# Optimization experiments

Measured on AMD Instinct MI355X. Metric: run time of the kernel, lower is better.

## Reference

```python
import jax, jax.numpy as jnp
import numpy as np
from jax import lax

B, T, H, H1 = 128, 512, 256, 128


def setup_inputs() -> dict:
    key = jax.random.key(0)
    ks = jax.random.split(key, 9)
    s = 1.0 / np.sqrt(H)  # torch LSTM/Linear init scale (uniform), use scaled normal for simplicity
    return {
        "x": jax.random.normal(ks[0], (B, T, 1), dtype=jnp.float32),
        "W_ih": jax.random.normal(ks[1], (4 * H, 1), dtype=jnp.float32) * s,
        "W_hh": jax.random.normal(ks[2], (4 * H, H), dtype=jnp.float32) * s,
        "b_ih": jax.random.normal(ks[3], (4 * H,), dtype=jnp.float32) * s,
        "b_hh": jax.random.normal(ks[4], (4 * H,), dtype=jnp.float32) * s,
        "W1": jax.random.normal(ks[5], (H1, H), dtype=jnp.float32) * s,
        "b1": jax.random.normal(ks[6], (H1,), dtype=jnp.float32) * s,
        "W2": jax.random.normal(ks[7], (1, H1), dtype=jnp.float32) / np.sqrt(H1),
        "b2": jax.random.normal(ks[8], (1,), dtype=jnp.float32) / np.sqrt(H1),
    }


def _lstm_last_hidden(x, W_ih, W_hh, b_ih, b_hh):
    # Precompute input contribution for all timesteps: [B,T,4H]
    xg = jnp.einsum("bti,gi->btg", x, W_ih) + (b_ih + b_hh)
    Bv, Hv = x.shape[0], W_hh.shape[1]
    h0 = jnp.zeros((Bv, Hv), dtype=x.dtype)
    c0 = jnp.zeros((Bv, Hv), dtype=x.dtype)

    def step(carry, xg_t):
        h, c = carry
        gates = xg_t + h @ W_hh.T  # [B,4H]
        i, f, g, o = jnp.split(gates, 4, axis=-1)  # torch gate order: i,f,g,o
        i = jax.nn.sigmoid(i)
        f = jax.nn.sigmoid(f)
        g = jnp.tanh(g)
        o = jax.nn.sigmoid(o)
        c = f * c + i * g
        h = o * jnp.tanh(c)
        return (h, c), None

    (h_last, _), _ = lax.scan(step, (h0, c0), jnp.swapaxes(xg, 0, 1))
    return h_last  # == lstm output at t=T-1 (x[:, -1, :] in torch)


def reference(x, W_ih, W_hh, b_ih, b_hh, W1, b1, W2, b2):
    h = _lstm_last_hidden(x, W_ih, W_hh, b_ih, b_hh)  # [B,H]
    y = jax.nn.relu(h @ W1.T + b1) @ W2.T + b2  # [B,1]
    return y
```

## Files before the change

kernel.cpp:

```cpp
#include <hip/hip_runtime.h>

#define TT 512
#define HH 256

typedef _Float16 half2t __attribute__((ext_vector_type(2)));

__device__ __forceinline__ float dot2acc(unsigned w, unsigned h, float acc) {
#if __has_builtin(__builtin_amdgcn_fdot2)
    return __builtin_amdgcn_fdot2(__builtin_bit_cast(half2t, w),
                                  __builtin_bit_cast(half2t, h), acc, false);
#else
    union U { unsigned u; _Float16 f[2]; };
    U uw, uh; uw.u = w; uh.u = h;
    acc = __builtin_fmaf((float)uw.f[0], (float)uh.f[0], acc);
    acc = __builtin_fmaf((float)uw.f[1], (float)uh.f[1], acc);
    return acc;
#endif
}

__device__ __forceinline__ unsigned packh2(float a, float b) {
    union U { _Float16 f[2]; unsigned u; } r;
    r.f[0] = (_Float16)a; r.f[1] = (_Float16)b;
    return r.u;
}

#define AGPR_W(dst, src) \
    asm volatile("v_accvgpr_write_b32 %0, %1" : "=a"(dst) : "v"(src))
#define AGPR_R(dst, src) \
    asm("v_accvgpr_read_b32 %0, %1" : "=v"(dst) : "a"(src))

__device__ __forceinline__ float qsum4(float v) {
    int a = __builtin_amdgcn_mov_dpp(__builtin_bit_cast(int, v), 0xB1, 0xF, 0xF, true);
    float r = v + __builtin_bit_cast(float, a);
    int b = __builtin_amdgcn_mov_dpp(__builtin_bit_cast(int, r), 0x4E, 0xF, 0xF, true);
    return r + __builtin_bit_cast(float, b);
}

__global__ __launch_bounds__(1024)
__attribute__((amdgpu_waves_per_eu(4, 4)))
void lstm_single(
    const float* __restrict__ x,
    const float* __restrict__ W_ih,
    const float* __restrict__ W_hh,
    const float* __restrict__ b_ih,
    const float* __restrict__ b_hh,
    const float* __restrict__ W1,
    const float* __restrict__ b1,
    const float* __restrict__ W2,
    const float* __restrict__ b2,
    float* __restrict__ out)
{
    const int b = blockIdx.x;
    const int j = threadIdx.x;
    const int e = j >> 2;
    const int s = j & 3;

    __shared__ __align__(16) unsigned wl[9][1024][4];
    __shared__ __align__(16) unsigned hbuf[2][140];
    __shared__ float h32[HH];
    __shared__ float x_lds[TT];
    __shared__ float red[128];

    unsigned wag[64];
    unsigned wv[28];
    #pragma unroll
    for (int g = 0; g < 4; ++g) {
        const float* pR = W_hh + (size_t)(g * 256 + e) * HH + 64 * s;
        #pragma unroll
        for (int k = 0; k < 16; ++k) {
            unsigned pw = packh2(pR[2 * k], pR[2 * k + 1]);
            AGPR_W(wag[g * 16 + k], pw);
        }
        #pragma unroll
        for (int k = 0; k < 7; ++k)
            wv[g * 7 + k] = packh2(pR[2 * (16 + k)], pR[2 * (16 + k) + 1]);
    }
    #pragma unroll
    for (int k = 0; k < 28; ++k)
        asm volatile("" : "+v"(wv[k]));
    #pragma unroll
    for (int u = 0; u < 9; ++u) {
        #pragma unroll
        for (int c2 = 0; c2 < 4; ++c2) {
            const int m = 4 * u + c2;
            const int g = m / 9, k = 23 + m % 9;
            const float* pR = W_hh + (size_t)(g * 256 + e) * HH + 64 * s;
            wl[u][j][c2] = packh2(pR[2 * k], pR[2 * k + 1]);
        }
    }

    float wih[4], bias[4];
    #pragma unroll
    for (int g = 0; g < 4; ++g) {
        const int R = g * 256 + e;
        wih[g]  = W_ih[R];
        bias[g] = b_ih[R] + b_hh[R];
    }

    if (j < TT) x_lds[j] = x[(size_t)b * TT + j];
    if (j < 140) { hbuf[0][j] = 0u; hbuf[1][j] = 0u; }
    float c = 0.0f;
    __syncthreads();

    for (int t = 0; t < TT; ++t) {
        const int p  = t & 1;
        const int pn = p ^ 1;
        const float xv = x_lds[t];
        const unsigned* hb = &hbuf[p][36 * s];
        float acc[4] = {0.f, 0.f, 0.f, 0.f};

        #pragma unroll
        for (int i = 0; i < 4; ++i) {
            uint4 hq = *reinterpret_cast<const uint4*>(&hb[4 * i]);
            #pragma unroll
            for (int g = 0; g < 4; ++g) {
                unsigned w0, w1, w2, w3;
                AGPR_R(w0, wag[g * 16 + 4 * i + 0]);
                AGPR_R(w1, wag[g * 16 + 4 * i + 1]);
                AGPR_R(w2, wag[g * 16 + 4 * i + 2]);
                AGPR_R(w3, wag[g * 16 + 4 * i + 3]);
                acc[g] = dot2acc(w0, hq.x, acc[g]);
                acc[g] = dot2acc(w1, hq.y, acc[g]);
                acc[g] = dot2acc(w2, hq.z, acc[g]);
                acc[g] = dot2acc(w3, hq.w, acc[g]);
            }
        }
        uint4 h4 = *reinterpret_cast<const uint4*>(&hb[16]);
        uint4 h5 = *reinterpret_cast<const uint4*>(&hb[20]);
        #pragma unroll
        for (int g = 0; g < 4; ++g) {
            acc[g] = dot2acc(wv[g * 7 + 0], h4.x, acc[g]);
            acc[g] = dot2acc(wv[g * 7 + 1], h4.y, acc[g]);
            acc[g] = dot2acc(wv[g * 7 + 2], h4.z, acc[g]);
            acc[g] = dot2acc(wv[g * 7 + 3], h4.w, acc[g]);
            acc[g] = dot2acc(wv[g * 7 + 4], h5.x, acc[g]);
            acc[g] = dot2acc(wv[g * 7 + 5], h5.y, acc[g]);
            acc[g] = dot2acc(wv[g * 7 + 6], h5.z, acc[g]);
        }
        uint4 h6 = *reinterpret_cast<const uint4*>(&hb[24]);
        uint4 h7 = *reinterpret_cast<const uint4*>(&hb[28]);
        const unsigned hw[9] = {h5.w, h6.x, h6.y, h6.z, h6.w,
                                h7.x, h7.y, h7.z, h7.w};
        #pragma unroll
        for (int u = 0; u < 9; ++u) {
            uint4 wq = *reinterpret_cast<const uint4*>(&wl[u][j][0]);
            { const int m = 4*u+0; acc[m/9] = dot2acc(wq.x, hw[m%9], acc[m/9]); }
            { const int m = 4*u+1; acc[m/9] = dot2acc(wq.y, hw[m%9], acc[m/9]); }
            { const int m = 4*u+2; acc[m/9] = dot2acc(wq.z, hw[m%9], acc[m/9]); }
            { const int m = 4*u+3; acc[m/9] = dot2acc(wq.w, hw[m%9], acc[m/9]); }
        }

        float gi = qsum4(acc[0]) + __builtin_fmaf(xv, wih[0], bias[0]);
        float gf = qsum4(acc[1]) + __builtin_fmaf(xv, wih[1], bias[1]);
        float gg = qsum4(acc[2]) + __builtin_fmaf(xv, wih[2], bias[2]);
        float go = qsum4(acc[3]) + __builtin_fmaf(xv, wih[3], bias[3]);

        gi = __builtin_amdgcn_rcpf(1.f + __expf(-gi));
        gf = __builtin_amdgcn_rcpf(1.f + __expf(-gf));
        go = __builtin_amdgcn_rcpf(1.f + __expf(-go));
        gg = 2.f * __builtin_amdgcn_rcpf(1.f + __expf(-2.f * gg)) - 1.f;
        c = __builtin_fmaf(gf, c, gi * gg);
        float th = 2.f * __builtin_amdgcn_rcpf(1.f + __expf(-2.f * c)) - 1.f;
        float hn = go * th;

        if ((e >> 6) == s)
            reinterpret_cast<unsigned short*>(&hbuf[pn][0])[e + 8 * s] =
                __builtin_bit_cast(unsigned short, (_Float16)hn);
        if (s == 0) h32[e] = hn;
        __syncthreads();
    }

    if (j < 128) {
        const float4* w1p = reinterpret_cast<const float4*>(W1 + (size_t)j * HH);
        const float4* hp  = reinterpret_cast<const float4*>(h32);
        float s0 = 0.f, s1 = 0.f, s2 = 0.f, s3 = 0.f;
        #pragma unroll
        for (int k = 0; k < 64; ++k) {
            float4 wv4 = w1p[k], hv = hp[k];
            s0 = __builtin_fmaf(wv4.x, hv.x, s0);
            s1 = __builtin_fmaf(wv4.y, hv.y, s1);
            s2 = __builtin_fmaf(wv4.z, hv.z, s2);
            s3 = __builtin_fmaf(wv4.w, hv.w, s3);
        }
        float rv = fmaxf((s0 + s1) + (s2 + s3) + b1[j], 0.f);
        red[j] = rv * W2[j];
    }
    __syncthreads();
    if (j == 0) {
        float y = b2[0];
        #pragma unroll 4
        for (int k = 0; k < 128; ++k) y += red[k];
        out[b] = y;
    }
}

extern "C" void kernel_launch(void* const* d_in, const int* in_sizes, int n_in,
                              void* d_out, int out_size, void* d_ws, size_t ws_size,
                              hipStream_t stream) {
    const float* x    = (const float*)d_in[0];
    const float* W_ih = (const float*)d_in[1];
    const float* W_hh = (const float*)d_in[2];
    const float* b_ih = (const float*)d_in[3];
    const float* b_hh = (const float*)d_in[4];
    const float* W1   = (const float*)d_in[5];
    const float* b1   = (const float*)d_in[6];
    const float* W2   = (const float*)d_in[7];
    const float* b2   = (const float*)d_in[8];
    float* out = (float*)d_out;

    lstm_single<<<128, 1024, 0, stream>>>(x, W_ih, W_hh, b_ih, b_hh,
                                          W1, b1, W2, b2, out);
}
```

Measured before the change: 1.172 ms.

## Move LDS-resident recurrent weight tail into global workspace with register prefetch

The 144KB slice of packed fp16 W_hh that was held in shared memory is now written to a global workspace buffer and streamed back each timestep, software-pipelined through four uint4 registers loaded at the top of the loop. The aim is to free LDS and cut the cost of LDS reads inside the recurrence. In exchange every step depends on L2/L1 loads that sit on the serial critical path, and 100KB of dynamic shared memory is requested but never used. All blocks write identical data to the same workspace locations, which is benign but redundant.

```diff
diff --git a/kernel.cpp b/kernel.cpp
--- a/kernel.cpp
+++ b/kernel.cpp
@@ -35,6 +35,14 @@
     int b = __builtin_amdgcn_mov_dpp(__builtin_bit_cast(int, r), 0x4E, 0xF, 0xF, true);
     return r + __builtin_bit_cast(float, b);
 }
+
+#define TCONS(TQ, U)                                                          \
+    do {                                                                      \
+        acc[(4*(U)+0)/9] = dot2acc((TQ).x, hw[(4*(U)+0)%9], acc[(4*(U)+0)/9]); \
+        acc[(4*(U)+1)/9] = dot2acc((TQ).y, hw[(4*(U)+1)%9], acc[(4*(U)+1)/9]); \
+        acc[(4*(U)+2)/9] = dot2acc((TQ).z, hw[(4*(U)+2)%9], acc[(4*(U)+2)/9]); \
+        acc[(4*(U)+3)/9] = dot2acc((TQ).w, hw[(4*(U)+3)%9], acc[(4*(U)+3)/9]); \
+    } while (0)
 
 __global__ __launch_bounds__(1024)
 __attribute__((amdgpu_waves_per_eu(4, 4)))
@@ -48,14 +56,14 @@
     const float* __restrict__ b1,
     const float* __restrict__ W2,
     const float* __restrict__ b2,
-    float* __restrict__ out)
+    float* __restrict__ out,
+    uint4* __restrict__ wt)
 {
     const int b = blockIdx.x;
     const int j = threadIdx.x;
     const int e = j >> 2;
     const int s = j & 3;
 
-    __shared__ __align__(16) unsigned wl[9][1024][4];
     __shared__ __align__(16) unsigned hbuf[2][140];
     __shared__ float h32[HH];
     __shared__ float x_lds[TT];
@@ -78,15 +86,31 @@
     #pragma unroll
     for (int k = 0; k < 28; ++k)
         asm volatile("" : "+v"(wv[k]));
+
     #pragma unroll
     for (int u = 0; u < 9; ++u) {
-        #pragma unroll
-        for (int c2 = 0; c2 < 4; ++c2) {
-            const int m = 4 * u + c2;
-            const int g = m / 9, k = 23 + m % 9;
-            const float* pR = W_hh + (size_t)(g * 256 + e) * HH + 64 * s;
-            wl[u][j][c2] = packh2(pR[2 * k], pR[2 * k + 1]);
-        }
+        uint4 v;
+        {
+            const int m = 4 * u + 0, g = m / 9, k = 23 + m % 9;
+            const float* pR = W_hh + (size_t)(g * 256 + e) * HH + 64 * s;
+            v.x = packh2(pR[2 * k], pR[2 * k + 1]);
+        }
+        {
+            const int m = 4 * u + 1, g = m / 9, k = 23 + m % 9;
+            const float* pR = W_hh + (size_t)(g * 256 + e) * HH + 64 * s;
+            v.y = packh2(pR[2 * k], pR[2 * k + 1]);
+        }
+        {
+            const int m = 4 * u + 2, g = m / 9, k = 23 + m % 9;
+            const float* pR = W_hh + (size_t)(g * 256 + e) * HH + 64 * s;
+            v.z = packh2(pR[2 * k], pR[2 * k + 1]);
+        }
+        {
+            const int m = 4 * u + 3, g = m / 9, k = 23 + m % 9;
+            const float* pR = W_hh + (size_t)(g * 256 + e) * HH + 64 * s;
+            v.w = packh2(pR[2 * k], pR[2 * k + 1]);
+        }
+        wt[(size_t)j * 9 + u] = v;
     }
 
     float wih[4], bias[4];
@@ -102,9 +126,16 @@
     float c = 0.0f;
     __syncthreads();
 
+    const uint4* wtp = wt + (size_t)j * 9;
+
     for (int t = 0; t < TT; ++t) {
         const int p  = t & 1;
         const int pn = p ^ 1;
+        uint4 tq0 = wtp[0];
+        uint4 tq1 = wtp[1];
+        uint4 tq2 = wtp[2];
+        uint4 tq3 = wtp[3];
+
         const float xv = x_lds[t];
         const unsigned* hb = &hbuf[p][36 * s];
         float acc[4] = {0.f, 0.f, 0.f, 0.f};
@@ -141,14 +172,15 @@
         uint4 h7 = *reinterpret_cast<const uint4*>(&hb[28]);
         const unsigned hw[9] = {h5.w, h6.x, h6.y, h6.z, h6.w,
                                 h7.x, h7.y, h7.z, h7.w};
-        #pragma unroll
-        for (int u = 0; u < 9; ++u) {
-            uint4 wq = *reinterpret_cast<const uint4*>(&wl[u][j][0]);
-            { const int m = 4*u+0; acc[m/9] = dot2acc(wq.x, hw[m%9], acc[m/9]); }
-            { const int m = 4*u+1; acc[m/9] = dot2acc(wq.y, hw[m%9], acc[m/9]); }
-            { const int m = 4*u+2; acc[m/9] = dot2acc(wq.z, hw[m%9], acc[m/9]); }
-            { const int m = 4*u+3; acc[m/9] = dot2acc(wq.w, hw[m%9], acc[m/9]); }
-        }
+        TCONS(tq0, 0); tq0 = wtp[4];
+        TCONS(tq1, 1); tq1 = wtp[5];
+        TCONS(tq2, 2); tq2 = wtp[6];
+        TCONS(tq3, 3); tq3 = wtp[7];
+        TCONS(tq0, 4); tq0 = wtp[8];
+        TCONS(tq1, 5);
+        TCONS(tq2, 6);
+        TCONS(tq3, 7);
+        TCONS(tq0, 8);
 
         float gi = qsum4(acc[0]) + __builtin_fmaf(xv, wih[0], bias[0]);
         float gf = qsum4(acc[1]) + __builtin_fmaf(xv, wih[1], bias[1]);
@@ -207,7 +239,8 @@
     const float* W2   = (const float*)d_in[7];
     const float* b2   = (const float*)d_in[8];
     float* out = (float*)d_out;
-
-    lstm_single<<<128, 1024, 0, stream>>>(x, W_ih, W_hh, b_ih, b_hh,
-                                          W1, b1, W2, b2, out);
-}
+    uint4* wt  = (uint4*)d_ws;
+
+    lstm_single<<<128, 1024, 100 * 1024, stream>>>(x, W_ih, W_hh, b_ih, b_hh,
+                                                   W1, b1, W2, b2, out, wt);
+}
```

Result: slower. 3.020 ms (+157.7%).
